# Kernel optimization log

Hardware: AMD Instinct MI355X
Metric: run time of the kernel (lower is better)

Reference implementation:

```python
import jax, jax.numpy as jnp
import numpy as np

H = 4        # heads
C = 128      # out_channels per head (concat=False)
D = 128      # hidden_dim
N = 50000    # nodes
E = 800000   # edges (before self loops)
SLOPE = 0.2  # leaky_relu negative slope (PyG default)


def setup_inputs() -> dict:
    key = jax.random.key(0)
    k0, k1, k2, k3, k4 = jax.random.split(key, 5)
    x = jax.random.normal(k0, (N, D), dtype=jnp.float32)
    edge_index = jax.random.randint(k1, (2, E), 0, N)
    W = jax.random.normal(k2, (D, H * C), dtype=jnp.float32) * (1.0 / np.sqrt(D))
    att_src = jax.random.normal(k3, (H, C), dtype=jnp.float32) * 0.1
    att_dst = jax.random.normal(k4, (H, C), dtype=jnp.float32) * 0.1
    bias = jnp.zeros((C,), dtype=jnp.float32)
    return {"x": x, "edge_index": edge_index, "W": W,
            "att_src": att_src, "att_dst": att_dst, "bias": bias}


def reference(x, edge_index, W, att_src, att_dst, bias):
    n = x.shape[0]
    # add self loops (add_self_loops=True)
    loop = jnp.arange(n, dtype=edge_index.dtype)
    src = jnp.concatenate([edge_index[0], loop])  # message sources
    dst = jnp.concatenate([edge_index[1], loop])  # aggregation targets

    h = (x @ W).reshape(n, H, C)                  # [N, H, C]
    a_src = jnp.einsum('nhc,hc->nh', h, att_src)  # [N, H]
    a_dst = jnp.einsum('nhc,hc->nh', h, att_dst)  # [N, H]

    # per-edge attention logits + leaky relu
    e = a_src[src] + a_dst[dst]                   # [Etot, H]
    e = jnp.where(e >= 0, e, SLOPE * e)

    # scatter-softmax over incoming edges of each dst node
    m = jax.ops.segment_max(e, dst, num_segments=n)      # [N, H]
    p = jnp.exp(e - m[dst])                              # [Etot, H]
    s = jax.ops.segment_sum(p, dst, num_segments=n)      # [N, H]
    alpha = p / s[dst]                                   # [Etot, H]

    # weighted scatter-aggregate of source features
    msg = alpha[:, :, None] * h[src]                     # [Etot, H, C]
    out = jax.ops.segment_sum(msg, dst, num_segments=n)  # [N, H, C]

    # concat=False -> mean over heads, then bias (dropout = identity in eval)
    return out.mean(axis=1) + bias
```

## Files before the change

### kernel.cpp

```cpp
#include <hip/hip_runtime.h>
#include <math.h>

typedef __attribute__((ext_vector_type(8))) short bf16x8;
typedef __attribute__((ext_vector_type(4))) float f32x4;

#define MAXDEG 128

__device__ __forceinline__ float lrelu(float v) { return v >= 0.0f ? v : 0.2f * v; }

__device__ __forceinline__ unsigned short f2bf(float f) {
    unsigned u = __builtin_bit_cast(unsigned, f);
    unsigned r = (u + 0x7fffu + ((u >> 16) & 1u)) >> 16;
    return (unsigned short)r;
}
__device__ __forceinline__ float bflo(unsigned u) { return __builtin_bit_cast(float, u << 16); }
__device__ __forceinline__ float bfhi(unsigned u) { return __builtin_bit_cast(float, u & 0xffff0000u); }
__device__ __forceinline__ unsigned pack2bf(float a, float b) {
    return (unsigned)f2bf(a) | ((unsigned)f2bf(b) << 16);
}

__global__ __launch_bounds__(256) void wa_zero(const float* __restrict__ W,
                                               const float* __restrict__ att_src,
                                               const float* __restrict__ att_dst,
                                               float* __restrict__ Wa,
                                               int* __restrict__ deg, int N) {
    const int t = threadIdx.x;
    if ((int)blockIdx.x < 64) {
        int gid = (int)blockIdx.x * 256 + t;
        int o = gid >> 4, l16 = gid & 15;
        int d = o >> 3, j = o & 7;
        int hd = j & 3;
        const float* att = (j < 4) ? att_src : att_dst;
        const float* wp = &W[d * 512 + hd * 128 + l16 * 8];
        const float* ap = &att[hd * 128 + l16 * 8];
        float4 w0 = *(const float4*)wp, w1 = *(const float4*)(wp + 4);
        float4 a0 = *(const float4*)ap, a1 = *(const float4*)(ap + 4);
        float s = w0.x * a0.x + w0.y * a0.y + w0.z * a0.z + w0.w * a0.w +
                  w1.x * a1.x + w1.y * a1.y + w1.z * a1.z + w1.w * a1.w;
        #pragma unroll
        for (int off = 1; off < 16; off <<= 1) s += __shfl_xor(s, off);
        if (l16 == 0) Wa[o] = s;
    } else {
        int i = ((int)blockIdx.x - 64) * 256 + t;
        if (i < N) deg[i] = 0;
    }
}

__global__ __launch_bounds__(256) void prep(const float* __restrict__ x,
                                            const float* __restrict__ W,
                                            const float* __restrict__ Wa,
                                            const int* __restrict__ esrc,
                                            const int* __restrict__ edst, int E,
                                            unsigned* __restrict__ xb32,
                                            unsigned short* __restrict__ Wt,
                                            float* __restrict__ a_src4,
                                            float* __restrict__ a_dst4,
                                            int* __restrict__ deg,
                                            unsigned short* __restrict__ csr16,
                                            int N, int nA, int nE) {
    const int t = threadIdx.x;
    const int bid = (int)blockIdx.x;

    int section, sid;
    if (bid < 2 * nE) {
        section = (bid & 1) ? 0 : 2;
        sid = bid >> 1;
    } else if (bid < nE + nA) {
        section = 0;
        sid = nE + (bid - 2 * nE);
    } else {
        section = 1;
        sid = bid - nE - nA;
    }

    if (section == 0) {
        const int wid = t >> 6, l = t & 63;
        float wa0[8], wa1[8];
        {
            const float4* wp = (const float4*)&Wa[(l * 2) * 8];
            float4 a0 = wp[0], a1 = wp[1], b0 = wp[2], b1 = wp[3];
            wa0[0] = a0.x; wa0[1] = a0.y; wa0[2] = a0.z; wa0[3] = a0.w;
            wa0[4] = a1.x; wa0[5] = a1.y; wa0[6] = a1.z; wa0[7] = a1.w;
            wa1[0] = b0.x; wa1[1] = b0.y; wa1[2] = b0.z; wa1[3] = b0.w;
            wa1[4] = b1.x; wa1[5] = b1.y; wa1[6] = b1.z; wa1[7] = b1.w;
        }
        const int sel = l & 7;
        #pragma unroll
        for (int nd = 0; nd < 4; nd++) {
            const int n = sid * 16 + wid * 4 + nd;
            if (n >= N) continue;
            float2 xv = *(const float2*)&x[(size_t)n * 128 + l * 2];
            xb32[(size_t)n * 64 + l] = pack2bf(xv.x, xv.y);
            float acc[8];
            #pragma unroll
            for (int j = 0; j < 8; j++) acc[j] = fmaf(xv.x, wa0[j], xv.y * wa1[j]);
            #pragma unroll
            for (int off = 1; off < 8; off <<= 1) {
                #pragma unroll
                for (int j = 0; j < 8; j++) acc[j] += __shfl_xor(acc[j], off);
            }
            float a01 = (sel & 1) ? acc[1] : acc[0];
            float a23 = (sel & 1) ? acc[3] : acc[2];
            float a45 = (sel & 1) ? acc[5] : acc[4];
            float a67 = (sel & 1) ? acc[7] : acc[6];
            float a03 = (sel & 2) ? a23 : a01;
            float a47 = (sel & 2) ? a67 : a45;
            float v = (sel & 4) ? a47 : a03;
            #pragma unroll
            for (int off = 8; off < 64; off <<= 1) v += __shfl_xor(v, off);
            if (l < 8) {
                if (l < 4) a_src4[n * 4 + l] = v;
                else       a_dst4[n * 4 + (l - 4)] = v;
            }
        }
    } else if (section == 1) {
        int id = sid * 256 + t;
        int k = id >> 9, n = id & 511;
        Wt[n * 128 + k] = f2bf(W[k * 512 + n]);
    } else {
        int base = sid * 2048 + t;
        #pragma unroll
        for (int k = 0; k < 8; k++) {
            int i = base + k * 256;
            if (i < E) {
                int d = edst[i];
                int pos = atomicAdd(&deg[d], 1);
                if (pos < MAXDEG) csr16[(size_t)pos * N + d] = (unsigned short)esrc[i];
            }
        }
    }
}

#define LDA 136

__global__ __launch_bounds__(256, 3) void gemm_mfma(const unsigned short* __restrict__ xb,
                                                    const unsigned short* __restrict__ Wt,
                                                    unsigned short* __restrict__ h2, int N) {
    __shared__ unsigned short Cs[128 * LDA];

    const int brow = blockIdx.y * 128;
    const int bcol = blockIdx.x * 128;
    const int t = threadIdx.x;
    const int wid = t >> 6, l = t & 63;
    const int wr = wid >> 1, wc = wid & 1;
    const int r = l & 15, g = l >> 4;

    const unsigned short* ap[4];
    const unsigned short* bp[4];
    #pragma unroll
    for (int m = 0; m < 4; m++)
        ap[m] = &xb[(size_t)(brow + wr * 64 + m * 16 + r) * 128 + g * 8];
    #pragma unroll
    for (int n = 0; n < 4; n++)
        bp[n] = &Wt[(size_t)(bcol + wc * 64 + n * 16 + r) * 128 + g * 8];

    f32x4 zero4 = {0.f, 0.f, 0.f, 0.f};
    f32x4 acc[4][4];
    #pragma unroll
    for (int m = 0; m < 4; m++)
        #pragma unroll
        for (int n = 0; n < 4; n++) acc[m][n] = zero4;

    #pragma unroll
    for (int ks = 0; ks < 4; ks++) {
        bf16x8 a[4], b[4];
        #pragma unroll
        for (int m = 0; m < 4; m++) a[m] = *(const bf16x8*)(ap[m] + ks * 32);
        #pragma unroll
        for (int n = 0; n < 4; n++) b[n] = *(const bf16x8*)(bp[n] + ks * 32);
        #pragma unroll
        for (int m = 0; m < 4; m++)
            #pragma unroll
            for (int n = 0; n < 4; n++)
                acc[m][n] = __builtin_amdgcn_mfma_f32_16x16x32_bf16(a[m], b[n], acc[m][n], 0, 0, 0);
    }

    #pragma unroll
    for (int m = 0; m < 4; m++) {
        #pragma unroll
        for (int n = 0; n < 4; n++) {
            #pragma unroll
            for (int j = 0; j < 4; j++) {
                int row = wr * 64 + m * 16 + g * 4 + j;
                int col = wc * 64 + n * 16 + r;
                Cs[row * LDA + col] = f2bf(acc[m][n][j]);
            }
        }
    }
    __syncthreads();
    #pragma unroll
    for (int i = 0; i < 8; i++) {
        int idx = t + 256 * i;
        int row = idx >> 4, c = idx & 15;
        if (brow + row < N) {
            uint4 v = *(const uint4*)&Cs[row * LDA + c * 8];
            *(uint4*)&h2[(size_t)(brow + row) * 512 + bcol + c * 8] = v;
        }
    }
}

#define ACCUM(p, v)                                                            \
    {                                                                          \
        acc[0] = fmaf(p, bflo(v.x), acc[0]);                                   \
        acc[1] = fmaf(p, bfhi(v.x), acc[1]);                                   \
        acc[2] = fmaf(p, bflo(v.y), acc[2]);                                   \
        acc[3] = fmaf(p, bfhi(v.y), acc[3]);                                   \
        acc[4] = fmaf(p, bflo(v.z), acc[4]);                                   \
        acc[5] = fmaf(p, bfhi(v.z), acc[5]);                                   \
        acc[6] = fmaf(p, bflo(v.w), acc[6]);                                   \
        acc[7] = fmaf(p, bfhi(v.w), acc[7]);                                   \
    }

__global__ __launch_bounds__(256) void aggregate(const unsigned short* __restrict__ h2,
                                                 const float* __restrict__ a_src4,
                                                 const float* __restrict__ a_dst4,
                                                 const int* __restrict__ deg,
                                                 const unsigned short* __restrict__ csr16,
                                                 const float* __restrict__ bias,
                                                 float* __restrict__ out, int N) {
    int wid = (blockIdx.x * 256 + threadIdx.x) >> 6;
    int l = threadIdx.x & 63;
    if (wid >= N) return;
    const int n = wid;
    const int hd = l >> 4;

    const float ad_my = a_dst4[n * 4 + hd];
    float acc[8];
    float ssum;
    {
        float p = __expf(lrelu(a_src4[n * 4 + hd] + ad_my));
        ssum = p;
        uint4 v = *(const uint4*)&h2[(size_t)n * 512 + l * 8];
        acc[0] = p * bflo(v.x); acc[1] = p * bfhi(v.x);
        acc[2] = p * bflo(v.y); acc[3] = p * bfhi(v.y);
        acc[4] = p * bflo(v.z); acc[5] = p * bfhi(v.z);
        acc[6] = p * bflo(v.w); acc[7] = p * bfhi(v.w);
    }

    int dg = deg[n];
    if (dg > MAXDEG) dg = MAXDEG;
    const int nb = dg >> 3;

    int sidx[8];
    if (nb > 0) {
        #pragma unroll
        for (int j = 0; j < 8; j++) sidx[j] = csr16[(size_t)j * N + n];
    }
    for (int b = 0; b < nb; b++) {
        int nsidx[8];
        if (b + 1 < nb) {
            #pragma unroll
            for (int j = 0; j < 8; j++)
                nsidx[j] = csr16[(size_t)((b + 1) * 8 + j) * N + n];
        }
        float lg[8];
        #pragma unroll
        for (int j = 0; j < 8; j++) lg[j] = a_src4[sidx[j] * 4 + hd];
        uint4 hv[8];
        #pragma unroll
        for (int j = 0; j < 8; j++) hv[j] = *(const uint4*)&h2[(size_t)sidx[j] * 512 + l * 8];
        float p[8];
        #pragma unroll
        for (int j = 0; j < 8; j++) {
            p[j] = __expf(lrelu(lg[j] + ad_my));
            ssum += p[j];
        }
        #pragma unroll
        for (int j = 0; j < 8; j++) ACCUM(p[j], hv[j]);
        #pragma unroll
        for (int j = 0; j < 8; j++) sidx[j] = nsidx[j];
    }
    for (int e = nb * 8; e < dg; e++) {
        int s = csr16[(size_t)e * N + n];
        float le = a_src4[s * 4 + hd];
        uint4 v = *(const uint4*)&h2[(size_t)s * 512 + l * 8];
        float p = __expf(lrelu(le + ad_my));
        ssum += p;
        ACCUM(p, v);
    }

    float inv = 1.0f / (4.0f * ssum);
    #pragma unroll
    for (int j = 0; j < 8; j++) acc[j] *= inv;
    #pragma unroll
    for (int off = 16; off < 64; off <<= 1) {
        #pragma unroll
        for (int j = 0; j < 8; j++) acc[j] += __shfl_xor(acc[j], off);
    }
    if (l < 16) {
        const float* bp = &bias[l * 8];
        float4 b0 = *(const float4*)bp;
        float4 b1 = *(const float4*)(bp + 4);
        float* op = &out[(size_t)n * 128 + l * 8];
        *(float4*)op = make_float4(acc[0] + b0.x, acc[1] + b0.y, acc[2] + b0.z, acc[3] + b0.w);
        *(float4*)(op + 4) = make_float4(acc[4] + b1.x, acc[5] + b1.y, acc[6] + b1.z, acc[7] + b1.w);
    }
}

extern "C" void kernel_launch(void* const* d_in, const int* in_sizes, int n_in,
                              void* d_out, int out_size, void* d_ws, size_t ws_size,
                              hipStream_t stream) {
    const float* x = (const float*)d_in[0];
    const int* ei = (const int*)d_in[1];
    const float* W = (const float*)d_in[2];
    const float* att_src = (const float*)d_in[3];
    const float* att_dst = (const float*)d_in[4];
    const float* bias = (const float*)d_in[5];
    float* out = (float*)d_out;

    const int N = in_sizes[0] / 128;
    const int E = in_sizes[1] / 2;
    const int* esrc = ei;
    const int* edst = ei + E;

    char* ws = (char*)d_ws;
    size_t off = 0;
    auto alloc = [&](size_t bytes) {
        void* p = ws + off;
        off = (off + bytes + 511) & ~(size_t)511;
        return p;
    };
    unsigned short* h2 = (unsigned short*)alloc((size_t)N * 512 * 2);
    unsigned short* xb = (unsigned short*)alloc((size_t)N * 128 * 2);
    unsigned short* Wt = (unsigned short*)alloc((size_t)512 * 128 * 2);
    float* Wa = (float*)alloc((size_t)1024 * 4);
    float* a_src4 = (float*)alloc((size_t)N * 16);
    float* a_dst4 = (float*)alloc((size_t)N * 16);
    int* deg = (int*)alloc((size_t)N * 4);
    unsigned short* csr16 = (unsigned short*)alloc((size_t)MAXDEG * N * 2);

    const int nZ = (N + 255) / 256;
    wa_zero<<<64 + nZ, 256, 0, stream>>>(W, att_src, att_dst, Wa, deg, N);

    const int nA = (N + 15) / 16;
    const int nE = (E + 2047) / 2048;
    prep<<<nA + 256 + nE, 256, 0, stream>>>(x, W, Wa, esrc, edst, E, (unsigned*)xb, Wt,
                                            a_src4, a_dst4, deg, csr16, N, nA, nE);

    dim3 gg(4, (N + 127) / 128);
    gemm_mfma<<<gg, 256, 0, stream>>>(xb, Wt, h2, N);

    int nwave_blocks = (N * 64 + 255) / 256;
    aggregate<<<nwave_blocks, 256, 0, stream>>>(h2, a_src4, a_dst4, deg, csr16, bias, out, N);
}
```

Before: 213.0 us.

## Fuse bf16 conversion and MFMA GEMM into prep kernel, move W transpose to setup

The x@W GEMM is folded into the prep kernel. Each 16-row block converts its x rows to bf16 in shared memory and immediately runs MFMA against the full 512-column Wt, so the intermediate xb buffer and one kernel launch are gone. The W transpose moves into the setup kernel so Wt is ready before prep runs. The cost is that each block now reads all of Wt straight from global or L2 for only 16 rows, which lowers reuse per block and raises shared memory use.

```diff
diff --git a/kernel.cpp b/kernel.cpp
--- a/kernel.cpp
+++ b/kernel.cpp
@@ -5,6 +5,8 @@
 typedef __attribute__((ext_vector_type(4))) float f32x4;
 
 #define MAXDEG 128
+#define LDXA 132
+#define LDC 520
 
 __device__ __forceinline__ float lrelu(float v) { return v >= 0.0f ? v : 0.2f * v; }
 
@@ -19,11 +21,12 @@
     return (unsigned)f2bf(a) | ((unsigned)f2bf(b) << 16);
 }
 
-__global__ __launch_bounds__(256) void wa_zero(const float* __restrict__ W,
-                                               const float* __restrict__ att_src,
-                                               const float* __restrict__ att_dst,
-                                               float* __restrict__ Wa,
-                                               int* __restrict__ deg, int N) {
+__global__ __launch_bounds__(256) void setup(const float* __restrict__ W,
+                                             const float* __restrict__ att_src,
+                                             const float* __restrict__ att_dst,
+                                             float* __restrict__ Wa,
+                                             unsigned short* __restrict__ Wt,
+                                             int* __restrict__ deg, int N) {
     const int t = threadIdx.x;
     if ((int)blockIdx.x < 64) {
         int gid = (int)blockIdx.x * 256 + t;
@@ -40,24 +43,29 @@
         #pragma unroll
         for (int off = 1; off < 16; off <<= 1) s += __shfl_xor(s, off);
         if (l16 == 0) Wa[o] = s;
+    } else if ((int)blockIdx.x < 320) {
+        int id = ((int)blockIdx.x - 64) * 256 + t;
+        int k = id >> 9, n = id & 511;
+        Wt[n * 128 + k] = f2bf(W[k * 512 + n]);
     } else {
-        int i = ((int)blockIdx.x - 64) * 256 + t;
+        int i = ((int)blockIdx.x - 320) * 256 + t;
         if (i < N) deg[i] = 0;
     }
 }
 
-__global__ __launch_bounds__(256) void prep(const float* __restrict__ x,
-                                            const float* __restrict__ W,
-                                            const float* __restrict__ Wa,
-                                            const int* __restrict__ esrc,
-                                            const int* __restrict__ edst, int E,
-                                            unsigned* __restrict__ xb32,
-                                            unsigned short* __restrict__ Wt,
-                                            float* __restrict__ a_src4,
-                                            float* __restrict__ a_dst4,
-                                            int* __restrict__ deg,
-                                            unsigned short* __restrict__ csr16,
-                                            int N, int nA, int nE) {
+__global__ __launch_bounds__(256) void prep_gemm(const float* __restrict__ x,
+                                                 const float* __restrict__ Wa,
+                                                 const unsigned short* __restrict__ Wt,
+                                                 const int* __restrict__ esrc,
+                                                 const int* __restrict__ edst, int E,
+                                                 unsigned short* __restrict__ h2,
+                                                 float* __restrict__ a_src4,
+                                                 float* __restrict__ a_dst4,
+                                                 int* __restrict__ deg,
+                                                 unsigned short* __restrict__ csr16,
+                                                 int N, int nA, int nE) {
+    __shared__ unsigned short Xa[16 * LDXA];
+    __shared__ unsigned short Cs[16 * LDC];
     const int t = threadIdx.x;
     const int bid = (int)blockIdx.x;
 
@@ -65,16 +73,30 @@
     if (bid < 2 * nE) {
         section = (bid & 1) ? 0 : 2;
         sid = bid >> 1;
-    } else if (bid < nE + nA) {
+    } else {
         section = 0;
         sid = nE + (bid - 2 * nE);
-    } else {
-        section = 1;
-        sid = bid - nE - nA;
-    }
-
-    if (section == 0) {
-        const int wid = t >> 6, l = t & 63;
+    }
+
+    if (section == 2) {
+        int base = sid * 2048 + t;
+        #pragma unroll
+        for (int k = 0; k < 8; k++) {
+            int i = base + k * 256;
+            if (i < E) {
+                int d = edst[i];
+                int pos = atomicAdd(&deg[d], 1);
+                if (pos < MAXDEG) csr16[(size_t)pos * N + d] = (unsigned short)esrc[i];
+            }
+        }
+        return;
+    }
+
+    const int w = t >> 6, l = t & 63;
+    const int r = l & 15, g = l >> 4;
+    const int base = sid * 16;
+
+    {
         float wa0[8], wa1[8];
         {
             const float4* wp = (const float4*)&Wa[(l * 2) * 8];
@@ -87,10 +109,12 @@
         const int sel = l & 7;
         #pragma unroll
         for (int nd = 0; nd < 4; nd++) {
-            const int n = sid * 16 + wid * 4 + nd;
+            const int row = w * 4 + nd;
+            const int n = base + row;
+            float2 xv = make_float2(0.f, 0.f);
+            if (n < N) xv = *(const float2*)&x[(size_t)n * 128 + l * 2];
+            *(unsigned*)&Xa[row * LDXA + l * 2] = pack2bf(xv.x, xv.y);
             if (n >= N) continue;
-            float2 xv = *(const float2*)&x[(size_t)n * 128 + l * 2];
-            xb32[(size_t)n * 64 + l] = pack2bf(xv.x, xv.y);
             float acc[8];
             #pragma unroll
             for (int j = 0; j < 8; j++) acc[j] = fmaf(xv.x, wa0[j], xv.y * wa1[j]);
@@ -113,88 +137,45 @@
                 else       a_dst4[n * 4 + (l - 4)] = v;
             }
         }
-    } else if (section == 1) {
-        int id = sid * 256 + t;
-        int k = id >> 9, n = id & 511;
-        Wt[n * 128 + k] = f2bf(W[k * 512 + n]);
-    } else {
-        int base = sid * 2048 + t;
-        #pragma unroll
-        for (int k = 0; k < 8; k++) {
-            int i = base + k * 256;
-            if (i < E) {
-                int d = edst[i];
-                int pos = atomicAdd(&deg[d], 1);
-                if (pos < MAXDEG) csr16[(size_t)pos * N + d] = (unsigned short)esrc[i];
-            }
-        }
-    }
-}
-
-#define LDA 136
-
-__global__ __launch_bounds__(256, 3) void gemm_mfma(const unsigned short* __restrict__ xb,
-                                                    const unsigned short* __restrict__ Wt,
-                                                    unsigned short* __restrict__ h2, int N) {
-    __shared__ unsigned short Cs[128 * LDA];
-
-    const int brow = blockIdx.y * 128;
-    const int bcol = blockIdx.x * 128;
-    const int t = threadIdx.x;
-    const int wid = t >> 6, l = t & 63;
-    const int wr = wid >> 1, wc = wid & 1;
-    const int r = l & 15, g = l >> 4;
-
-    const unsigned short* ap[4];
-    const unsigned short* bp[4];
-    #pragma unroll
-    for (int m = 0; m < 4; m++)
-        ap[m] = &xb[(size_t)(brow + wr * 64 + m * 16 + r) * 128 + g * 8];
-    #pragma unroll
-    for (int n = 0; n < 4; n++)
-        bp[n] = &Wt[(size_t)(bcol + wc * 64 + n * 16 + r) * 128 + g * 8];
-
-    f32x4 zero4 = {0.f, 0.f, 0.f, 0.f};
-    f32x4 acc[4][4];
-    #pragma unroll
-    for (int m = 0; m < 4; m++)
-        #pragma unroll
-        for (int n = 0; n < 4; n++) acc[m][n] = zero4;
-
-    #pragma unroll
-    for (int ks = 0; ks < 4; ks++) {
-        bf16x8 a[4], b[4];
-        #pragma unroll
-        for (int m = 0; m < 4; m++) a[m] = *(const bf16x8*)(ap[m] + ks * 32);
-        #pragma unroll
-        for (int n = 0; n < 4; n++) b[n] = *(const bf16x8*)(bp[n] + ks * 32);
-        #pragma unroll
-        for (int m = 0; m < 4; m++)
-            #pragma unroll
-            for (int n = 0; n < 4; n++)
-                acc[m][n] = __builtin_amdgcn_mfma_f32_16x16x32_bf16(a[m], b[n], acc[m][n], 0, 0, 0);
-    }
-
-    #pragma unroll
-    for (int m = 0; m < 4; m++) {
-        #pragma unroll
-        for (int n = 0; n < 4; n++) {
+    }
+    __syncthreads();
+
+    {
+        f32x4 zero4 = {0.f, 0.f, 0.f, 0.f};
+        f32x4 acc[8];
+        #pragma unroll
+        for (int nf = 0; nf < 8; nf++) acc[nf] = zero4;
+
+        #pragma unroll
+        for (int ks = 0; ks < 4; ks++) {
+            bf16x8 a = *(const bf16x8*)&Xa[r * LDXA + ks * 32 + g * 8];
+            #pragma unroll
+            for (int nf = 0; nf < 8; nf++) {
+                int col = w * 128 + nf * 16 + r;
+                bf16x8 b = *(const bf16x8*)&Wt[(size_t)col * 128 + ks * 32 + g * 8];
+                acc[nf] = __builtin_amdgcn_mfma_f32_16x16x32_bf16(a, b, acc[nf], 0, 0, 0);
+            }
+        }
+
+        #pragma unroll
+        for (int nf = 0; nf < 8; nf++) {
             #pragma unroll
             for (int j = 0; j < 4; j++) {
-                int row = wr * 64 + m * 16 + g * 4 + j;
-                int col = wc * 64 + n * 16 + r;
-                Cs[row * LDA + col] = f2bf(acc[m][n][j]);
+                Cs[(g * 4 + j) * LDC + w * 128 + nf * 16 + r] = f2bf(acc[nf][j]);
             }
         }
     }
     __syncthreads();
-    #pragma unroll
-    for (int i = 0; i < 8; i++) {
-        int idx = t + 256 * i;
-        int row = idx >> 4, c = idx & 15;
-        if (brow + row < N) {
-            uint4 v = *(const uint4*)&Cs[row * LDA + c * 8];
-            *(uint4*)&h2[(size_t)(brow + row) * 512 + bcol + c * 8] = v;
+
+    {
+        const int row = t >> 4, c16 = t & 15;
+        if (base + row < N) {
+            #pragma unroll
+            for (int i = 0; i < 4; i++) {
+                int c = c16 * 4 + i;
+                uint4 v = *(const uint4*)&Cs[row * LDC + c * 8];
+                *(uint4*)&h2[(size_t)(base + row) * 512 + c * 8] = v;
+            }
         }
     }
 }
@@ -321,7 +302,6 @@
         return p;
     };
     unsigned short* h2 = (unsigned short*)alloc((size_t)N * 512 * 2);
-    unsigned short* xb = (unsigned short*)alloc((size_t)N * 128 * 2);
     unsigned short* Wt = (unsigned short*)alloc((size_t)512 * 128 * 2);
     float* Wa = (float*)alloc((size_t)1024 * 4);
     float* a_src4 = (float*)alloc((size_t)N * 16);
@@ -330,15 +310,12 @@
     unsigned short* csr16 = (unsigned short*)alloc((size_t)MAXDEG * N * 2);
 
     const int nZ = (N + 255) / 256;
-    wa_zero<<<64 + nZ, 256, 0, stream>>>(W, att_src, att_dst, Wa, deg, N);
+    setup<<<320 + nZ, 256, 0, stream>>>(W, att_src, att_dst, Wa, Wt, deg, N);
 
     const int nA = (N + 15) / 16;
     const int nE = (E + 2047) / 2048;
-    prep<<<nA + 256 + nE, 256, 0, stream>>>(x, W, Wa, esrc, edst, E, (unsigned*)xb, Wt,
-                                            a_src4, a_dst4, deg, csr16, N, nA, nE);
-
-    dim3 gg(4, (N + 127) / 128);
-    gemm_mfma<<<gg, 256, 0, stream>>>(xb, Wt, h2, N);
+    prep_gemm<<<nA + nE, 256, 0, stream>>>(x, Wa, Wt, esrc, edst, E, h2,
+                                           a_src4, a_dst4, deg, csr16, N, nA, nE);
 
     int nwave_blocks = (N * 64 + 255) / 256;
     aggregate<<<nwave_blocks, 256, 0, stream>>>(h2, a_src4, a_dst4, deg, csr16, bias, out, N);
```

Result: slower. 220.9 us (+3.7%).
